# Performance work log

Hardware: AMD Instinct MI355X
Metric: run time of the kernel (lower is better)

## Reference

```python
import jax, jax.numpy as jnp
import numpy as np

B, S, D = 1, 2048, 4096
HQ, HK, HD = 32, 8, 128


def setup_inputs() -> dict:
    key = jax.random.key(0)
    ks = jax.random.split(key, 6)
    x = jax.random.normal(ks[0], (B, S, D), jnp.float32) * 0.02
    wq = jax.random.normal(ks[1], (D, HQ * HD), jnp.float32) * 0.02
    wk = jax.random.normal(ks[2], (D, HK * HD), jnp.float32) * 0.02
    wv = jax.random.normal(ks[3], (D, HK * HD), jnp.float32) * 0.02
    wo = jax.random.normal(ks[4], (HQ * HD, D), jnp.float32) * 0.02
    # canonical RoPE frequencies: theta = 10000
    inv_freq = 1.0 / (10000.0 ** (jnp.arange(0, HD, 2, dtype=jnp.float32) / HD))  # [HD/2]
    t = jnp.arange(S, dtype=jnp.float32)
    ang = jnp.outer(t, inv_freq)  # [S, HD/2]
    return {
        "x": x,
        "freqs_cos": jnp.cos(ang),
        "freqs_sin": jnp.sin(ang),
        "wq": wq, "wk": wk, "wv": wv, "wo": wo,
    }


def _rope(t, cos, sin):
    # t: [B, S, H, HD]; pairs are consecutive elements (view_as_complex semantics)
    tr = t.reshape(*t.shape[:-1], HD // 2, 2)
    t0, t1 = tr[..., 0], tr[..., 1]
    c = cos[None, :, None, :]
    s = sin[None, :, None, :]
    o0 = t0 * c - t1 * s
    o1 = t0 * s + t1 * c
    return jnp.stack([o0, o1], axis=-1).reshape(t.shape)


def reference(x, freqs_cos, freqs_sin, wq, wk, wv, wo):
    b, s, _ = x.shape
    g = HQ // HK  # GQA group size
    xq = (x @ wq).reshape(b, s, HQ, HD)
    xk = (x @ wk).reshape(b, s, HK, HD)
    xv = (x @ wv).reshape(b, s, HK, HD)
    xq = _rope(xq, freqs_cos, freqs_sin)
    xk = _rope(xk, freqs_cos, freqs_sin)
    scale = 1.0 / jnp.sqrt(jnp.float32(HD))
    xqg = xq.reshape(b, s, HK, g, HD)
    # scores: [b, HK, g, s_q, s_k]
    scores = jnp.einsum("bqkgd,bnkd->bkgqn", xqg, xk) * scale
    causal = jnp.tril(jnp.ones((s, s), dtype=bool))
    scores = jnp.where(causal[None, None, None, :, :], scores, -jnp.inf)
    p = jax.nn.softmax(scores, axis=-1)
    out = jnp.einsum("bkgqn,bnkd->bqkgd", p, xv).reshape(b, s, HQ * HD)
    return out @ wo
```

## Files before the change

kernel.cpp:

```cpp
#include <hip/hip_runtime.h>
#include <stdint.h>

typedef __bf16 bf16_t;
typedef bf16_t bf16x8 __attribute__((ext_vector_type(8)));
typedef float f32x4 __attribute__((ext_vector_type(4)));
typedef unsigned int u32;
typedef unsigned short u16;

#define DEV_INLINE __device__ __forceinline__

#define S_LEN 2048
#define D_MODEL 4096
#define HQ 32
#define HK 8
#define HD 128
#define NQKV 6144

DEV_INLINE u16 f2bf(float x) {
  union { float f; uint32_t u; } v; v.f = x;
  uint32_t r = v.u + 0x7FFFu + ((v.u >> 16) & 1u);
  return (u16)(r >> 16);
}
DEV_INLINE float bf2f(u16 x) {
  union { uint32_t u; float f; } v; v.u = ((uint32_t)x) << 16;
  return v.f;
}
DEV_INLINE u32 pack2bf(float a, float b) {
  return (u32)f2bf(a) | ((u32)f2bf(b) << 16);
}

DEV_INLINE void async_load16(const void* g, void* l) {
  __builtin_amdgcn_global_load_lds(
      (const __attribute__((address_space(1))) u32*)g,
      (__attribute__((address_space(3))) u32*)l, 16, 0, 0);
}

DEV_INLINE f32x4 mfma16(bf16x8 a, bf16x8 b, f32x4 c) {
  return __builtin_amdgcn_mfma_f32_16x16x32_bf16(a, b, c, 0, 0, 0);
}

__global__ void cvt_f32_bf16(const float* __restrict__ in, u16* __restrict__ out, int n) {
  int i = (blockIdx.x * blockDim.x + threadIdx.x) * 4;
  if (i >= n) return;
  float4 v = *(const float4*)(in + i);
  union { u16 s[4]; uint2 u; } o;
  o.s[0] = f2bf(v.x); o.s[1] = f2bf(v.y); o.s[2] = f2bf(v.z); o.s[3] = f2bf(v.w);
  *(uint2*)(out + i) = o.u;
}

__global__ void transpose_f32_bf16(const float* __restrict__ in, u16* __restrict__ out,
                                   int R, int C) {
  __shared__ float tile[32][33];
  int tx = threadIdx.x, ty = threadIdx.y;
  int c0 = blockIdx.x * 32, r0 = blockIdx.y * 32;
#pragma unroll
  for (int i = 0; i < 4; ++i)
    tile[ty + i * 8][tx] = in[(long)(r0 + ty + i * 8) * C + c0 + tx];
  __syncthreads();
#pragma unroll
  for (int i = 0; i < 4; ++i)
    out[(long)(c0 + ty + i * 8) * R + r0 + tx] = f2bf(tile[tx][ty + i * 8]);
}

__global__ void transpose_bf16(const u16* __restrict__ in, u16* __restrict__ out,
                               int R, int C, int ld_in, int col_off) {
  __shared__ u16 tile[32][33];
  int tx = threadIdx.x, ty = threadIdx.y;
  int c0 = blockIdx.x * 32, r0 = blockIdx.y * 32;
#pragma unroll
  for (int i = 0; i < 4; ++i)
    tile[ty + i * 8][tx] = in[(long)(r0 + ty + i * 8) * ld_in + col_off + c0 + tx];
  __syncthreads();
#pragma unroll
  for (int i = 0; i < 4; ++i)
    out[(long)(c0 + ty + i * 8) * R + r0 + tx] = tile[tx][ty + i * 8];
}

__global__ void rope_bf16(const u16* __restrict__ in, const float* __restrict__ cosb,
                          const float* __restrict__ sinb, u16* __restrict__ out,
                          int H, int ld_in, int col_off, float scale) {
  int idx = blockIdx.x * blockDim.x + threadIdx.x;
  int j = idx & 63;
  int sh = idx >> 6;
  int s = sh / H, h = sh - s * H;
  const u16* ip = in + (long)s * ld_in + col_off + h * HD;
  union { u32 u; u16 s2[2]; } v; v.u = *(const u32*)(ip + 2 * j);
  float q0 = bf2f(v.s2[0]), q1 = bf2f(v.s2[1]);
  float c = cosb[s * 64 + j], sn = sinb[s * 64 + j];
  union { u16 s2[2]; u32 u; } o;
  o.s2[0] = f2bf((q0 * c - q1 * sn) * scale);
  o.s2[1] = f2bf((q0 * sn + q1 * c) * scale);
  *(u32*)(out + (long)sh * HD + 2 * j) = o.u;
}

#define BARRIER() asm volatile("s_barrier" ::: "memory")
#define WAIT_VM(N) asm volatile("s_waitcnt vmcnt(" #N ")" ::: "memory")

template <int BN, bool BF16OUT>
__global__ __launch_bounds__(256, 2) void gemm_bdir(
    const u16* __restrict__ A, const u16* __restrict__ Bt, void* __restrict__ Cv,
    int N, int K) {
  constexpr int NF = BN / 64;
  __shared__ __attribute__((aligned(16))) u16 lds[4][128 * 32];

  const int tid = threadIdx.x;
  const int lane = tid & 63, wave = tid >> 6;
  const int quad = lane >> 4, l15 = lane & 15;

  const int gx = gridDim.x;
  const int bid = blockIdx.y * gx + blockIdx.x;
  const int cpx = (gx * gridDim.y) >> 3;
  const int sw = (bid & 7) * cpx + (bid >> 3);
  const int bn = sw % gx, bm = sw / gx;

  const long arow = (long)bm * 128, brow = (long)bn * BN;
  const int NT = K >> 5;

  const u16* asrc[2];
  int adst[2];
#pragma unroll
  for (int j = 0; j < 2; ++j) {
    int c = tid + j * 256;
    int row = c >> 2, cc = c & 3, cs = cc ^ ((row >> 1) & 3);
    asrc[j] = A + (arow + row) * (long)K + cs * 8;
    adst[j] = c * 8;
  }
  const u16* bptr[NF];
#pragma unroll
  for (int j = 0; j < NF; ++j)
    bptr[j] = Bt + (brow + wave * (NF * 16) + j * 16 + l15) * (long)K + quad * 8;

  auto stageA = [&](int ts) {
    const int k0 = ts * 32;
    u16* base = &lds[ts & 3][0];
#pragma unroll
    for (int j = 0; j < 2; ++j) async_load16(asrc[j] + k0, base + adst[j]);
  };

  f32x4 acc[8][NF] = {};
  bf16x8 b0[NF], b1[NF];

  stageA(0); stageA(1); stageA(2);
#pragma unroll
  for (int j = 0; j < NF; ++j) b0[j] = *(const bf16x8*)(bptr[j]);
  WAIT_VM(0);
  BARRIER();

#define GD_TILE(T, BR, BPRE)                                             \
  {                                                                      \
    if ((T) + 3 < NT) stageA((T) + 3);                                   \
    if ((T) + 1 < NT) {                                                  \
      _Pragma("unroll")                                                  \
      for (int j = 0; j < NF; ++j)                                       \
        BPRE[j] = *(const bf16x8*)(bptr[j] + ((T) + 1) * 32);            \
    }                                                                    \
    const u16* lbase = &lds[(T) & 3][0];                                 \
    __builtin_amdgcn_s_setprio(1);                                       \
    _Pragma("unroll")                                                    \
    for (int i = 0; i < 8; ++i) {                                        \
      int row = i * 16 + l15;                                            \
      bf16x8 af = *(const bf16x8*)(lbase + row * 32 +                    \
                                   ((quad ^ ((row >> 1) & 3)) * 8));     \
      _Pragma("unroll")                                                  \
      for (int j = 0; j < NF; ++j)                                       \
        acc[i][j] = mfma16(af, BR[j], acc[i][j]);                        \
    }                                                                    \
    __builtin_amdgcn_s_setprio(0);                                       \
    BARRIER();                                                           \
  }

  for (int t = 0; t < NT; t += 2) {
    GD_TILE(t, b0, b1);
    GD_TILE(t + 1, b1, b0);
  }
#undef GD_TILE

#pragma unroll
  for (int i = 0; i < 8; ++i) {
    const long row = (long)bm * 128 + i * 16 + quad * 4;
#pragma unroll
    for (int j = 0; j < NF; ++j) {
      const int col = bn * BN + wave * (NF * 16) + j * 16 + l15;
      if constexpr (BF16OUT) {
        u16* C = (u16*)Cv;
#pragma unroll
        for (int r = 0; r < 4; ++r) C[(row + r) * N + col] = f2bf(acc[i][j][r]);
      } else {
        float* C = (float*)Cv;
#pragma unroll
        for (int r = 0; r < 4; ++r) C[(row + r) * N + col] = acc[i][j][r];
      }
    }
  }
}

#define NEG_INF -1e30f
__global__ __launch_bounds__(256, 2) void attn_fwd(
    const u16* __restrict__ Qb, const u16* __restrict__ Kb,
    const u16* __restrict__ Vt, u16* __restrict__ Ob) {
  __shared__ __attribute__((aligned(16))) u16 Ks[2][64 * 128];
  __shared__ __attribute__((aligned(16))) u16 Vs[2][128 * 64];
  __shared__ __attribute__((aligned(16))) u16 Pts[4][16 * 64];
  const int tid = threadIdx.x;
  const int lane = tid & 63, wave = tid >> 6;
  const int quad = lane >> 4, l15 = lane & 15;
  const int lin = blockIdx.y * gridDim.x + blockIdx.x;
  const int h = lin & 31;
  const int pp = (lin >> 5) & 7;
  const int u = (lin >> 8) ? 15 - pp : pp;
  const int hk = h >> 2;
  const int swz = 2 * (l15 & 7);
  const int nt = 2 * (u + 1);

  bf16x8 qf[2][4];
#pragma unroll
  for (int n = 0; n < 2; ++n) {
    const u16* qrow = Qb + (long)(u * 128 + wave * 32 + n * 16 + l15) * (HQ * HD)
                      + h * HD + quad * 8;
#pragma unroll
    for (int ks = 0; ks < 4; ++ks) qf[n][ks] = *(const bf16x8*)(qrow + ks * 32);
  }

  auto stage = [&](int t) {
    const int b = t & 1;
#pragma unroll
    for (int it = 0; it < 4; ++it) {
      int c = tid + it * 256;
      int row = c >> 4, cc = c & 15, cs = cc ^ (row & 15);
      async_load16(Kb + (long)(t * 64 + row) * (HK * HD) + hk * HD + cs * 8,
                   (u16*)&Ks[b][0] + c * 8);
    }
#pragma unroll
    for (int it = 0; it < 4; ++it) {
      int c = tid + it * 256;
      int row = c >> 3, cc = c & 7, cs = cc ^ (row & 7);
      async_load16(Vt + (long)(hk * HD + row) * S_LEN + t * 64 + cs * 8,
                   (u16*)&Vs[b][0] + c * 8);
    }
  };

  float m_run[2] = {NEG_INF, NEG_INF}, l_run[2] = {0.f, 0.f};
  f32x4 oacc[8][2] = {};

  stage(0);
  __syncthreads();

  for (int t = 0; t < nt; ++t) {
    const int cur = t & 1;
    if (t + 1 < nt) stage(t + 1);

    if (t * 64 <= u * 128 + wave * 32 + 31) {
      f32x4 sc[4][2] = {};
      __builtin_amdgcn_s_setprio(1);
#pragma unroll
      for (int ks = 0; ks < 4; ++ks)
#pragma unroll
        for (int tj = 0; tj < 4; ++tj) {
          int row = tj * 16 + l15;
          bf16x8 kf = *(const bf16x8*)(&Ks[cur][0] + row * 128
                                       + (((ks * 4 + quad) ^ (row & 15)) * 8));
          sc[tj][0] = mfma16(kf, qf[0][ks], sc[tj][0]);
          sc[tj][1] = mfma16(kf, qf[1][ks], sc[tj][1]);
        }
      __builtin_amdgcn_s_setprio(0);

      const bool diag = (t >= 2 * u);
      const int kbase = t * 64 - u * 128;
#pragma unroll
      for (int n = 0; n < 2; ++n) {
        int qloc = wave * 32 + n * 16 + l15;
        if (diag) {
#pragma unroll
          for (int tj = 0; tj < 4; ++tj)
#pragma unroll
            for (int r = 0; r < 4; ++r)
              if (kbase + tj * 16 + quad * 4 + r > qloc) sc[tj][n][r] = NEG_INF;
        }
        float m = NEG_INF;
#pragma unroll
        for (int tj = 0; tj < 4; ++tj)
#pragma unroll
          for (int r = 0; r < 4; ++r) m = fmaxf(m, sc[tj][n][r]);
        m = fmaxf(m, __shfl_xor(m, 16));
        m = fmaxf(m, __shfl_xor(m, 32));
        if (!__all(m - m_run[n] <= 8.0f)) {
          float mnew = fmaxf(m_run[n], m);
          float alpha = __expf(m_run[n] - mnew);
          m_run[n] = mnew;
          l_run[n] *= alpha;
#pragma unroll
          for (int tj = 0; tj < 8; ++tj) oacc[tj][n] *= alpha;
        }
        float rs = 0.f;
#pragma unroll
        for (int tj = 0; tj < 4; ++tj)
#pragma unroll
          for (int r = 0; r < 4; ++r) {
            float p = __expf(sc[tj][n][r] - m_run[n]);
            sc[tj][n][r] = p;
            rs += p;
          }
        rs += __shfl_xor(rs, 16);
        rs += __shfl_xor(rs, 32);
        l_run[n] += rs;
      }

      u16* pw = &Pts[wave][0];
      bf16x8 pf0[2], pf1[2];
#pragma unroll
      for (int tj = 0; tj < 4; ++tj) {
        union { u32 w[2]; uint2 u2; } pk;
        pk.w[0] = pack2bf(sc[tj][0][0], sc[tj][0][1]);
        pk.w[1] = pack2bf(sc[tj][0][2], sc[tj][0][3]);
        *(uint2*)(pw + l15 * 64 + (((tj * 4 + quad) ^ swz) * 4)) = pk.u2;
      }
      __asm__ volatile("s_waitcnt lgkmcnt(0)" ::: "memory");
#pragma unroll
      for (int ks = 0; ks < 2; ++ks)
        pf0[ks] = *(const bf16x8*)(pw + l15 * 64 + (((ks * 8 + quad * 2) ^ swz) * 4));
      __asm__ volatile("s_waitcnt lgkmcnt(0)" ::: "memory");
#pragma unroll
      for (int tj = 0; tj < 4; ++tj) {
        union { u32 w[2]; uint2 u2; } pk;
        pk.w[0] = pack2bf(sc[tj][1][0], sc[tj][1][1]);
        pk.w[1] = pack2bf(sc[tj][1][2], sc[tj][1][3]);
        *(uint2*)(pw + l15 * 64 + (((tj * 4 + quad) ^ swz) * 4)) = pk.u2;
      }
      __asm__ volatile("s_waitcnt lgkmcnt(0)" ::: "memory");
#pragma unroll
      for (int ks = 0; ks < 2; ++ks)
        pf1[ks] = *(const bf16x8*)(pw + l15 * 64 + (((ks * 8 + quad * 2) ^ swz) * 4));

      __builtin_amdgcn_s_setprio(1);
#pragma unroll
      for (int ks = 0; ks < 2; ++ks)
#pragma unroll
        for (int tj = 0; tj < 8; ++tj) {
          int row = tj * 16 + l15;
          bf16x8 vf = *(const bf16x8*)(&Vs[cur][0] + row * 64
                                       + (((ks * 4 + quad) ^ (row & 7)) * 8));
          oacc[tj][0] = mfma16(vf, pf0[ks], oacc[tj][0]);
          oacc[tj][1] = mfma16(vf, pf1[ks], oacc[tj][1]);
        }
      __builtin_amdgcn_s_setprio(0);
    }

    __syncthreads();
  }

#pragma unroll
  for (int n = 0; n < 2; ++n) {
    float inv_l = 1.0f / l_run[n];
    long grow = u * 128 + wave * 32 + n * 16 + l15;
#pragma unroll
    for (int tj = 0; tj < 8; ++tj) {
      int gcol = h * HD + tj * 16 + quad * 4;
      union { u32 w[2]; uint2 u2; } pk;
      pk.w[0] = pack2bf(oacc[tj][n][0] * inv_l, oacc[tj][n][1] * inv_l);
      pk.w[1] = pack2bf(oacc[tj][n][2] * inv_l, oacc[tj][n][3] * inv_l);
      *(uint2*)(Ob + grow * (HQ * HD) + gcol) = pk.u2;
    }
  }
}

#define MB (1024L * 1024L)

extern "C" void kernel_launch(void* const* d_in, const int* in_sizes, int n_in,
                              void* d_out, int out_size, void* d_ws, size_t ws_size,
                              hipStream_t stream) {
  const float* x    = (const float*)d_in[0];
  const float* fcos = (const float*)d_in[1];
  const float* fsin = (const float*)d_in[2];
  const float* wq   = (const float*)d_in[3];
  const float* wk   = (const float*)d_in[4];
  const float* wv   = (const float*)d_in[5];
  const float* wo   = (const float*)d_in[6];
  float* out = (float*)d_out;

  char* ws = (char*)d_ws;
  u16* wt    = (u16*)(ws + 0 * MB);
  u16* xb    = (u16*)(ws + 48 * MB);
  u16* QKVb  = (u16*)(ws + 64 * MB);
  u16* Qb    = (u16*)(ws + 88 * MB);
  u16* Kb    = (u16*)(ws + 104 * MB);
  u16* Vt    = (u16*)(ws + 108 * MB);
  u16* attnb = (u16*)(ws + 112 * MB);

  const int M = S_LEN, D = D_MODEL;

  cvt_f32_bf16<<<(M * D) / 1024, 256, 0, stream>>>(x, xb, M * D);

  transpose_f32_bf16<<<dim3(D / 32, D / 32), dim3(32, 8), 0, stream>>>(wq, wt, D, HQ * HD);
  transpose_f32_bf16<<<dim3((HK * HD) / 32, D / 32), dim3(32, 8), 0, stream>>>(
      wk, wt + (long)(HQ * HD) * D, D, HK * HD);
  transpose_f32_bf16<<<dim3((HK * HD) / 32, D / 32), dim3(32, 8), 0, stream>>>(
      wv, wt + (long)(HQ * HD + HK * HD) * D, D, HK * HD);

  gemm_bdir<192, true><<<dim3(NQKV / 192, M / 128), 256, 0, stream>>>(
      xb, wt, QKVb, NQKV, D);

  rope_bf16<<<(M * HQ * 64) / 256, 256, 0, stream>>>(
      QKVb, fcos, fsin, Qb, HQ, NQKV, 0, 0.08838834764831845f);
  rope_bf16<<<(M * HK * 64) / 256, 256, 0, stream>>>(
      QKVb, fcos, fsin, Kb, HK, NQKV, HQ * HD, 1.0f);
  transpose_bf16<<<dim3((HK * HD) / 32, M / 32), dim3(32, 8), 0, stream>>>(
      QKVb, Vt, M, HK * HD, NQKV, HQ * HD + HK * HD);

  attn_fwd<<<dim3(16, HQ), 256, 0, stream>>>(Qb, Kb, Vt, attnb);

  transpose_f32_bf16<<<dim3(D / 32, D / 32), dim3(32, 8), 0, stream>>>(wo, wt, HQ * HD, D);
  gemm_bdir<128, false><<<dim3(D / 128, M / 128), 256, 0, stream>>>(
      attnb, wt, out, D, HQ * HD);
}
```

Measured before the change: 548.6 us.

## Stage B tiles through LDS with double buffering and widen transpose tiles

The GEMM used to load B fragments straight from global memory into registers while A went through a 4-deep async LDS ring. Now both A and B tiles are staged into a 2-deep LDS double buffer with swizzled async loads, and B fragments are read from LDS. This is meant to coalesce the B loads, at the cost of a shallower prefetch depth and a full vmcnt wait plus barrier every K-step. The weight transpose kernels also move from 32x32 to 64x64 tiles with 64x4 thread blocks.

```diff
diff --git a/kernel.cpp b/kernel.cpp
--- a/kernel.cpp
+++ b/kernel.cpp
@@ -50,16 +50,16 @@
 
 __global__ void transpose_f32_bf16(const float* __restrict__ in, u16* __restrict__ out,
                                    int R, int C) {
-  __shared__ float tile[32][33];
+  __shared__ float tile[64][65];
   int tx = threadIdx.x, ty = threadIdx.y;
-  int c0 = blockIdx.x * 32, r0 = blockIdx.y * 32;
-#pragma unroll
-  for (int i = 0; i < 4; ++i)
-    tile[ty + i * 8][tx] = in[(long)(r0 + ty + i * 8) * C + c0 + tx];
+  int c0 = blockIdx.x * 64, r0 = blockIdx.y * 64;
+#pragma unroll
+  for (int i = 0; i < 16; ++i)
+    tile[ty + i * 4][tx] = in[(long)(r0 + ty + i * 4) * C + c0 + tx];
   __syncthreads();
 #pragma unroll
-  for (int i = 0; i < 4; ++i)
-    out[(long)(c0 + ty + i * 8) * R + r0 + tx] = f2bf(tile[tx][ty + i * 8]);
+  for (int i = 0; i < 16; ++i)
+    out[(long)(c0 + ty + i * 4) * R + r0 + tx] = f2bf(tile[tx][ty + i * 4]);
 }
 
 __global__ void transpose_bf16(const u16* __restrict__ in, u16* __restrict__ out,
@@ -97,11 +97,14 @@
 #define WAIT_VM(N) asm volatile("s_waitcnt vmcnt(" #N ")" ::: "memory")
 
 template <int BN, bool BF16OUT>
-__global__ __launch_bounds__(256, 2) void gemm_bdir(
+__global__ __launch_bounds__(256, 2) void gemm_db(
     const u16* __restrict__ A, const u16* __restrict__ Bt, void* __restrict__ Cv,
     int N, int K) {
   constexpr int NF = BN / 64;
-  __shared__ __attribute__((aligned(16))) u16 lds[4][128 * 32];
+  constexpr int BPT = (BN * 4) / 256;
+  constexpr int LDSU = (128 + BN) * 32;
+
+  __shared__ __attribute__((aligned(16))) u16 lds[2][LDSU];
 
   const int tid = threadIdx.x;
   const int lane = tid & 63, wave = tid >> 6;
@@ -116,64 +119,53 @@
   const long arow = (long)bm * 128, brow = (long)bn * BN;
   const int NT = K >> 5;
 
-  const u16* asrc[2];
-  int adst[2];
-#pragma unroll
-  for (int j = 0; j < 2; ++j) {
-    int c = tid + j * 256;
-    int row = c >> 2, cc = c & 3, cs = cc ^ ((row >> 1) & 3);
-    asrc[j] = A + (arow + row) * (long)K + cs * 8;
-    adst[j] = c * 8;
-  }
-  const u16* bptr[NF];
-#pragma unroll
-  for (int j = 0; j < NF; ++j)
-    bptr[j] = Bt + (brow + wave * (NF * 16) + j * 16 + l15) * (long)K + quad * 8;
-
-  auto stageA = [&](int ts) {
+  auto stage = [&](int ts) {
     const int k0 = ts * 32;
-    u16* base = &lds[ts & 3][0];
-#pragma unroll
-    for (int j = 0; j < 2; ++j) async_load16(asrc[j] + k0, base + adst[j]);
+    u16* base = &lds[ts & 1][0];
+#pragma unroll
+    for (int j = 0; j < 2; ++j) {
+      int c = tid + j * 256;
+      int row = c >> 2, cc = c & 3, cs = cc ^ ((row >> 1) & 3);
+      async_load16(A + (arow + row) * (long)K + k0 + cs * 8, base + c * 8);
+    }
+#pragma unroll
+    for (int j = 0; j < BPT; ++j) {
+      int c = tid + j * 256;
+      int row = c >> 2, cc = c & 3, cs = cc ^ ((row >> 1) & 3);
+      async_load16(Bt + (brow + row) * (long)K + k0 + cs * 8,
+                   base + 4096 + c * 8);
+    }
   };
+  auto rdfrag = [&](const u16* base, int row) -> bf16x8 {
+    return *(const bf16x8*)(base + row * 32 + ((quad ^ ((row >> 1) & 3)) * 8));
+  };
 
   f32x4 acc[8][NF] = {};
-  bf16x8 b0[NF], b1[NF];
-
-  stageA(0); stageA(1); stageA(2);
-#pragma unroll
-  for (int j = 0; j < NF; ++j) b0[j] = *(const bf16x8*)(bptr[j]);
+
+  stage(0);
   WAIT_VM(0);
   BARRIER();
 
-#define GD_TILE(T, BR, BPRE)                                             \
-  {                                                                      \
-    if ((T) + 3 < NT) stageA((T) + 3);                                   \
-    if ((T) + 1 < NT) {                                                  \
-      _Pragma("unroll")                                                  \
-      for (int j = 0; j < NF; ++j)                                       \
-        BPRE[j] = *(const bf16x8*)(bptr[j] + ((T) + 1) * 32);            \
-    }                                                                    \
-    const u16* lbase = &lds[(T) & 3][0];                                 \
-    __builtin_amdgcn_s_setprio(1);                                       \
-    _Pragma("unroll")                                                    \
-    for (int i = 0; i < 8; ++i) {                                        \
-      int row = i * 16 + l15;                                            \
-      bf16x8 af = *(const bf16x8*)(lbase + row * 32 +                    \
-                                   ((quad ^ ((row >> 1) & 3)) * 8));     \
-      _Pragma("unroll")                                                  \
-      for (int j = 0; j < NF; ++j)                                       \
-        acc[i][j] = mfma16(af, BR[j], acc[i][j]);                        \
-    }                                                                    \
-    __builtin_amdgcn_s_setprio(0);                                       \
-    BARRIER();                                                           \
+  for (int t = 0; t < NT; ++t) {
+    if (t + 1 < NT) stage(t + 1);
+    const u16* Ab = &lds[t & 1][0];
+    const u16* Bb = Ab + 4096;
+    bf16x8 bfr[NF];
+#pragma unroll
+    for (int j = 0; j < NF; ++j)
+      bfr[j] = rdfrag(Bb, wave * (NF * 16) + j * 16 + l15);
+    __builtin_amdgcn_s_setprio(1);
+#pragma unroll
+    for (int i = 0; i < 8; ++i) {
+      bf16x8 af = rdfrag(Ab, i * 16 + l15);
+#pragma unroll
+      for (int j = 0; j < NF; ++j)
+        acc[i][j] = mfma16(af, bfr[j], acc[i][j]);
+    }
+    __builtin_amdgcn_s_setprio(0);
+    WAIT_VM(0);
+    BARRIER();
   }
-
-  for (int t = 0; t < NT; t += 2) {
-    GD_TILE(t, b0, b1);
-    GD_TILE(t + 1, b1, b0);
-  }
-#undef GD_TILE
 
 #pragma unroll
   for (int i = 0; i < 8; ++i) {
@@ -390,13 +382,13 @@
 
   cvt_f32_bf16<<<(M * D) / 1024, 256, 0, stream>>>(x, xb, M * D);
 
-  transpose_f32_bf16<<<dim3(D / 32, D / 32), dim3(32, 8), 0, stream>>>(wq, wt, D, HQ * HD);
-  transpose_f32_bf16<<<dim3((HK * HD) / 32, D / 32), dim3(32, 8), 0, stream>>>(
+  transpose_f32_bf16<<<dim3(D / 64, D / 64), dim3(64, 4), 0, stream>>>(wq, wt, D, HQ * HD);
+  transpose_f32_bf16<<<dim3((HK * HD) / 64, D / 64), dim3(64, 4), 0, stream>>>(
       wk, wt + (long)(HQ * HD) * D, D, HK * HD);
-  transpose_f32_bf16<<<dim3((HK * HD) / 32, D / 32), dim3(32, 8), 0, stream>>>(
+  transpose_f32_bf16<<<dim3((HK * HD) / 64, D / 64), dim3(64, 4), 0, stream>>>(
       wv, wt + (long)(HQ * HD + HK * HD) * D, D, HK * HD);
 
-  gemm_bdir<192, true><<<dim3(NQKV / 192, M / 128), 256, 0, stream>>>(
+  gemm_db<192, true><<<dim3(NQKV / 192, M / 128), 256, 0, stream>>>(
       xb, wt, QKVb, NQKV, D);
 
   rope_bf16<<<(M * HQ * 64) / 256, 256, 0, stream>>>(
@@ -408,7 +400,7 @@
 
   attn_fwd<<<dim3(16, HQ), 256, 0, stream>>>(Qb, Kb, Vt, attnb);
 
-  transpose_f32_bf16<<<dim3(D / 32, D / 32), dim3(32, 8), 0, stream>>>(wo, wt, HQ * HD, D);
-  gemm_bdir<128, false><<<dim3(D / 128, M / 128), 256, 0, stream>>>(
+  transpose_f32_bf16<<<dim3(D / 64, D / 64), dim3(64, 4), 0, stream>>>(wo, wt, HQ * HD, D);
+  gemm_db<128, false><<<dim3(D / 128, M / 128), 256, 0, stream>>>(
       attnb, wt, out, D, HQ * HD);
 }
```

Measured after the change: 507.3 us. 1.08x faster.
